# Kernel optimization log

Hardware: AMD Instinct MI355X
Metric: run time of the kernel (lower is better)

Reference implementation:

```python
import jax, jax.numpy as jnp
import numpy as np

jax.config.update("jax_enable_x64", True)  # hash arithmetic needs 64-bit ints

P = 56598313          # RzLinear.P (prime for the hash)
INPUT_DIM = 4096
OUTPUT_DIM = 4096
COMPRESS_RATIO = 0.0625
HASH_SIZE = int(INPUT_DIM * OUTPUT_DIM * COMPRESS_RATIO)  # 1,048,576
N_TOKENS = 8192


def setup_inputs() -> dict:
    key = jax.random.key(0)
    kx, kw, kr = jax.random.split(key, 3)
    x = jax.random.normal(kx, (N_TOKENS, INPUT_DIM), dtype=jnp.float32)
    hashed_weight = jax.random.normal(kw, (HASH_SIZE,), dtype=jnp.float32) * 0.02
    # _generate_random_numbers: [P, r1, r2, r3] with r_i forced even via r + r % 2
    r = jax.random.randint(kr, (3,), 0, P, dtype=jnp.int64)
    r = r + r % 2
    random_numbers = jnp.concatenate([jnp.array([P], dtype=jnp.int64), r])
    bias = jnp.zeros((OUTPUT_DIM,), dtype=jnp.float32)
    return {"x": x, "hashed_weight": hashed_weight,
            "random_numbers": random_numbers, "bias": bias}


def _hash_indices(random_numbers):
    # ROBE-Z hash (chunk_size=1): idx[k, n] = ((k*r3 + n*r2 + r1) % P) % HASH_SIZE
    r0 = random_numbers[0]
    r1 = random_numbers[1]
    r2 = random_numbers[2]
    r3 = random_numbers[3]
    k = jnp.arange(INPUT_DIM, dtype=jnp.int64)[:, None]   # (K, 1)
    n = jnp.arange(OUTPUT_DIM, dtype=jnp.int64)[None, :]  # (1, N)
    return ((k * r3 + n * r2 + r1) % r0) % HASH_SIZE       # (K, N)


def reference(x, hashed_weight, random_numbers, bias):
    idx = _hash_indices(random_numbers)
    W = hashed_weight[idx]          # gather-reconstructed (input_dim, output_dim)
    return x @ W + bias             # (N_TOKENS, output_dim)
```

## Files before the change

kernel.cpp:

```cpp
#include <hip/hip_runtime.h>
#include <stdint.h>


#define P_CONST 56598313u
#define HASH_MASK 0xFFFFFu
#define M_DIM 8192
#define N_DIM 4096
#define K_DIM 4096

typedef __attribute__((ext_vector_type(8))) short bf16x8;
typedef __attribute__((ext_vector_type(4))) float f32x4;

__device__ __forceinline__ unsigned short f2bf(float f) {
    unsigned int u = __float_as_uint(f);
    return (unsigned short)((u + 0x7FFFu + ((u >> 16) & 1u)) >> 16);
}

struct RN { unsigned long long r1, r2, r3; };

__device__ __forceinline__ RN decode_rn(const void* rn_raw) {
    RN o;
    const long long* rn64 = (const long long*)rn_raw;
    if (rn64[0] == 56598313LL) {
        o.r1 = (unsigned long long)rn64[1];
        o.r2 = (unsigned long long)rn64[2];
        o.r3 = (unsigned long long)rn64[3];
    } else {
        const int* rn32 = (const int*)rn_raw;
        o.r1 = (unsigned long long)(unsigned int)rn32[1];
        o.r2 = (unsigned long long)(unsigned int)rn32[2];
        o.r3 = (unsigned long long)(unsigned int)rn32[3];
    }
    return o;
}

__device__ __forceinline__ void load16(const void* g, void* l) {
    __builtin_amdgcn_global_load_lds(
        (const __attribute__((address_space(1))) void*)g,
        (__attribute__((address_space(3))) void*)l,
        16, 0, 0);
}

__global__ __launch_bounds__(256) void build_wt(const float* __restrict__ table,
                                                const void* __restrict__ rn_raw,
                                                unsigned short* __restrict__ Wt) {
    RN rn = decode_rn(rn_raw);
    const unsigned int stepu = (unsigned int)(rn.r3 % P_CONST);
    const unsigned int n = blockIdx.x;
    const unsigned long long base =
        ((unsigned long long)n * rn.r2 + rn.r1) % P_CONST;
    const int t = threadIdx.x;
#pragma unroll
    for (int e = 0; e < 2; ++e) {
        const int k0 = (t + e * 256) * 8;
        unsigned int cur =
            (unsigned int)((base + (unsigned long long)k0 * stepu) % P_CONST);
        union { unsigned short s[8]; uint4 v; } o;
#pragma unroll
        for (int i = 0; i < 8; ++i) {
            o.s[i] = f2bf(table[cur & HASH_MASK]);
            cur += stepu;
            if (cur >= P_CONST) cur -= P_CONST;
        }
        *(uint4*)(Wt + (size_t)n * K_DIM + k0) = o.v;
    }
}

__global__ __launch_bounds__(256) void cvt_x(const float* __restrict__ x,
                                             unsigned short* __restrict__ xb) {
    const size_t i8 = ((size_t)blockIdx.x * 256 + threadIdx.x) * 8;
    const float4 a = *(const float4*)(x + i8);
    const float4 b = *(const float4*)(x + i8 + 4);
    union { unsigned short s[8]; uint4 v; } o;
    o.s[0] = f2bf(a.x); o.s[1] = f2bf(a.y); o.s[2] = f2bf(a.z); o.s[3] = f2bf(a.w);
    o.s[4] = f2bf(b.x); o.s[5] = f2bf(b.y); o.s[6] = f2bf(b.z); o.s[7] = f2bf(b.w);
    *(uint4*)(xb + i8) = o.v;
}

__global__ __launch_bounds__(256) void gemm_bt(const unsigned short* __restrict__ A,
                                               const unsigned short* __restrict__ Bt,
                                               const float* __restrict__ bias,
                                               float* __restrict__ C) {
    __shared__ __align__(16) unsigned short lA[128 * 32];
    __shared__ __align__(16) unsigned short lB[128 * 32];
    const int t = threadIdx.x;
    const int m0 = blockIdx.y * 128;
    const int n0 = blockIdx.x * 128;
    const int lane = t & 63;
    const int w = t >> 6;
    const int wr = w >> 1, wc = w & 1;
    const int lm = lane & 15, q = lane >> 4;

    f32x4 acc[4][4] = {};

    for (int k0 = 0; k0 < K_DIM; k0 += 32) {
#pragma unroll
        for (int c = t; c < 512; c += 256) {
            const unsigned short* gp =
                A + (size_t)(m0 + (c >> 2)) * K_DIM + k0 + (c & 3) * 8;
            load16(gp, (char*)lA + (size_t)c * 16);
        }
#pragma unroll
        for (int c = t; c < 512; c += 256) {
            const unsigned short* gp =
                Bt + (size_t)(n0 + (c >> 2)) * K_DIM + k0 + (c & 3) * 8;
            load16(gp, (char*)lB + (size_t)c * 16);
        }
        __syncthreads();

        bf16x8 af[4], bfr[4];
#pragma unroll
        for (int i = 0; i < 4; ++i)
            af[i] = *(const bf16x8*)&lA[(wr * 64 + i * 16 + lm) * 32 + q * 8];
#pragma unroll
        for (int j = 0; j < 4; ++j)
            bfr[j] = *(const bf16x8*)&lB[(wc * 64 + j * 16 + lm) * 32 + q * 8];
#pragma unroll
        for (int i = 0; i < 4; ++i)
#pragma unroll
            for (int j = 0; j < 4; ++j)
                acc[i][j] = __builtin_amdgcn_mfma_f32_16x16x32_bf16(
                    af[i], bfr[j], acc[i][j], 0, 0, 0);
        __syncthreads();
    }

#pragma unroll
    for (int j = 0; j < 4; ++j) {
        const int col = n0 + wc * 64 + j * 16 + lm;
        const float bv = bias[col];
#pragma unroll
        for (int i = 0; i < 4; ++i) {
            const int row = m0 + wr * 64 + i * 16 + q * 4;
#pragma unroll
            for (int r = 0; r < 4; ++r)
                C[(size_t)(row + r) * N_DIM + col] = acc[i][j][r] + bv;
        }
    }
}

__global__ __launch_bounds__(256) void gemm_fused(const float* __restrict__ X,
                                                  const float* __restrict__ table,
                                                  const void* __restrict__ rn_raw,
                                                  const float* __restrict__ bias,
                                                  float* __restrict__ C) {
    RN rn = decode_rn(rn_raw);
    const unsigned int stepu = (unsigned int)(rn.r3 % P_CONST);
    const unsigned int step32 =
        (unsigned int)(((unsigned long long)stepu * 32ull) % P_CONST);

    __shared__ __align__(16) unsigned short lA[128 * 32];
    __shared__ __align__(16) unsigned short lB[128 * 32];
    const int t = threadIdx.x;
    const int m0 = blockIdx.y * 128;
    const int n0 = blockIdx.x * 128;
    const int lane = t & 63;
    const int w = t >> 6;
    const int wr = w >> 1, wc = w & 1;
    const int lm = lane & 15, q = lane >> 4;

    unsigned int curB[2];
    int rowB[2], colB[2];
#pragma unroll
    for (int e = 0; e < 2; ++e) {
        const int c = t + e * 256;
        rowB[e] = c >> 2;
        colB[e] = (c & 3) * 8;
        const unsigned long long base =
            ((unsigned long long)(n0 + rowB[e]) * rn.r2 + rn.r1) % P_CONST;
        curB[e] =
            (unsigned int)((base + (unsigned long long)colB[e] * stepu) % P_CONST);
    }

    f32x4 acc[4][4] = {};

    for (int k0 = 0; k0 < K_DIM; k0 += 32) {
#pragma unroll
        for (int c = t; c < 1024; c += 256) {
            const int row = c >> 3, col = (c & 7) * 4;
            const float4 v =
                *(const float4*)(X + (size_t)(m0 + row) * K_DIM + k0 + col);
            ushort4 o;
            o.x = f2bf(v.x); o.y = f2bf(v.y); o.z = f2bf(v.z); o.w = f2bf(v.w);
            *(ushort4*)&lA[row * 32 + col] = o;
        }
#pragma unroll
        for (int e = 0; e < 2; ++e) {
            unsigned int cur = curB[e];
            union { unsigned short s[8]; uint4 v; } o;
#pragma unroll
            for (int i = 0; i < 8; ++i) {
                o.s[i] = f2bf(table[cur & HASH_MASK]);
                cur += stepu;
                if (cur >= P_CONST) cur -= P_CONST;
            }
            curB[e] += step32;
            if (curB[e] >= P_CONST) curB[e] -= P_CONST;
            *(uint4*)&lB[rowB[e] * 32 + colB[e]] = o.v;
        }
        __syncthreads();

        bf16x8 af[4], bfr[4];
#pragma unroll
        for (int i = 0; i < 4; ++i)
            af[i] = *(const bf16x8*)&lA[(wr * 64 + i * 16 + lm) * 32 + q * 8];
#pragma unroll
        for (int j = 0; j < 4; ++j)
            bfr[j] = *(const bf16x8*)&lB[(wc * 64 + j * 16 + lm) * 32 + q * 8];
#pragma unroll
        for (int i = 0; i < 4; ++i)
#pragma unroll
            for (int j = 0; j < 4; ++j)
                acc[i][j] = __builtin_amdgcn_mfma_f32_16x16x32_bf16(
                    af[i], bfr[j], acc[i][j], 0, 0, 0);
        __syncthreads();
    }

#pragma unroll
    for (int j = 0; j < 4; ++j) {
        const int col = n0 + wc * 64 + j * 16 + lm;
        const float bv = bias[col];
#pragma unroll
        for (int i = 0; i < 4; ++i) {
            const int row = m0 + wr * 64 + i * 16 + q * 4;
#pragma unroll
            for (int r = 0; r < 4; ++r)
                C[(size_t)(row + r) * N_DIM + col] = acc[i][j][r] + bv;
        }
    }
}

extern "C" void kernel_launch(void* const* d_in, const int* in_sizes, int n_in,
                              void* d_out, int out_size, void* d_ws, size_t ws_size,
                              hipStream_t stream) {
    const float* x = (const float*)d_in[0];
    const float* hw = (const float*)d_in[1];
    const void* rn = d_in[2];
    const float* bias = (const float*)d_in[3];
    float* out = (float*)d_out;

    const size_t wt_bytes = (size_t)N_DIM * K_DIM * 2;
    const size_t xb_bytes = (size_t)M_DIM * K_DIM * 2;

    if (ws_size >= wt_bytes + xb_bytes) {
        unsigned short* Wt = (unsigned short*)d_ws;
        unsigned short* Xb = (unsigned short*)((char*)d_ws + wt_bytes);
        build_wt<<<N_DIM, 256, 0, stream>>>(hw, rn, Wt);
        cvt_x<<<(M_DIM * K_DIM) / (8 * 256), 256, 0, stream>>>(x, Xb);
        gemm_bt<<<dim3(N_DIM / 128, M_DIM / 128), 256, 0, stream>>>(Xb, Wt, bias, out);
    } else {
        gemm_fused<<<dim3(N_DIM / 128, M_DIM / 128), 256, 0, stream>>>(x, hw, rn, bias, out);
    }
}
```

Baseline: 591.0 us.

## Replace bf16 GEMM with 256x256-tile, 4-stage async-pipelined, swizzled LDS kernel

```diff
diff --git a/kernel.cpp b/kernel.cpp
--- a/kernel.cpp
+++ b/kernel.cpp
@@ -7,6 +7,8 @@
 #define M_DIM 8192
 #define N_DIM 4096
 #define K_DIM 4096
+#define BK 32
+#define KSTEPS (K_DIM / BK)
 
 typedef __attribute__((ext_vector_type(8))) short bf16x8;
 typedef __attribute__((ext_vector_type(4))) float f32x4;
@@ -77,10 +79,132 @@
     *(uint4*)(xb + i8) = o.v;
 }
 
-__global__ __launch_bounds__(256) void gemm_bt(const unsigned short* __restrict__ A,
-                                               const unsigned short* __restrict__ Bt,
-                                               const float* __restrict__ bias,
-                                               float* __restrict__ C) {
+__global__ __launch_bounds__(512, 2) void gemm_bt8(
+    const unsigned short* __restrict__ A,
+    const unsigned short* __restrict__ Bt,
+    const float* __restrict__ bias,
+    float* __restrict__ C) {
+    __shared__ __align__(16) unsigned short lA[4][256 * BK];
+    __shared__ __align__(16) unsigned short lB[4][256 * BK];
+
+    const int t = threadIdx.x;
+    const int bid0 = blockIdx.x;
+    const int sb = (bid0 & 7) * 64 + (bid0 >> 3);
+    const int m0 = (sb >> 4) * 256;
+    const int n0 = (sb & 15) * 256;
+
+    const int lane = t & 63;
+    const int wid = t >> 6;
+    const int wr = wid >> 2;
+    const int wc = wid & 3;
+    const int lm = lane & 15;
+    const int q = lane >> 4;
+    const int qswz = (q ^ ((lm >> 1) & 3)) << 4;
+
+    const int p0 = t * 16;
+    const int p1 = p0 + 8192;
+    const int l0 = p0 ^ ((p0 >> 3) & 0x30);
+    const int l1 = p1 ^ ((p1 >> 3) & 0x30);
+    const int r0 = l0 >> 6, c0 = (l0 & 63) >> 1;
+    const int r1 = l1 >> 6, c1 = (l1 & 63) >> 1;
+
+    const unsigned short* Abase = A + (size_t)m0 * K_DIM;
+    const unsigned short* Bbase = Bt + (size_t)n0 * K_DIM;
+
+    f32x4 acc[8][4] = {};
+
+#define STAGE_A(KS) do { const int b__ = (KS) & 3;                              \
+    load16(Abase + (size_t)r0 * K_DIM + (KS) * BK + c0, (char*)&lA[b__][0] + p0);\
+    load16(Abase + (size_t)r1 * K_DIM + (KS) * BK + c1, (char*)&lA[b__][0] + p1);\
+} while (0)
+#define STAGE_B(KS) do { const int b__ = (KS) & 3;                              \
+    load16(Bbase + (size_t)r0 * K_DIM + (KS) * BK + c0, (char*)&lB[b__][0] + p0);\
+    load16(Bbase + (size_t)r1 * K_DIM + (KS) * BK + c1, (char*)&lB[b__][0] + p1);\
+} while (0)
+
+#define STEP_BODY(KS, STG) do {                                                 \
+    __builtin_amdgcn_s_barrier();                                               \
+    asm volatile("" ::: "memory");                                              \
+    const char* bufA = (const char*)&lA[(KS) & 3][0];                           \
+    const char* bufB = (const char*)&lB[(KS) & 3][0];                           \
+    bf16x8 af[4], bfr[4];                                                       \
+    _Pragma("unroll")                                                           \
+    for (int i = 0; i < 4; ++i)                                                 \
+        af[i] = *(const bf16x8*)(bufA + (((wr * 128 + i * 16 + lm) << 6) | qswz));\
+    _Pragma("unroll")                                                           \
+    for (int j = 0; j < 4; ++j)                                                 \
+        bfr[j] = *(const bf16x8*)(bufB + (((wc * 64 + j * 16 + lm) << 6) | qswz));\
+    if (STG) STAGE_A((KS) + 3);                                                 \
+    asm volatile("s_waitcnt lgkmcnt(0)" ::: "memory");                          \
+    __builtin_amdgcn_sched_barrier(0);                                          \
+    __builtin_amdgcn_s_setprio(1);                                              \
+    _Pragma("unroll")                                                           \
+    for (int i = 0; i < 4; ++i)                                                 \
+        _Pragma("unroll")                                                       \
+        for (int j = 0; j < 4; ++j)                                             \
+            acc[i][j] = __builtin_amdgcn_mfma_f32_16x16x32_bf16(                \
+                af[i], bfr[j], acc[i][j], 0, 0, 0);                             \
+    __builtin_amdgcn_s_setprio(0);                                              \
+    __builtin_amdgcn_s_barrier();                                               \
+    asm volatile("" ::: "memory");                                              \
+    _Pragma("unroll")                                                           \
+    for (int i = 0; i < 4; ++i)                                                 \
+        af[i] = *(const bf16x8*)(bufA + (((wr * 128 + 64 + i * 16 + lm) << 6) | qswz));\
+    if (STG) STAGE_B((KS) + 3);                                                 \
+    asm volatile("s_waitcnt lgkmcnt(0)" ::: "memory");                          \
+    __builtin_amdgcn_sched_barrier(0);                                          \
+    __builtin_amdgcn_s_setprio(1);                                              \
+    _Pragma("unroll")                                                           \
+    for (int i = 0; i < 4; ++i)                                                 \
+        _Pragma("unroll")                                                       \
+        for (int j = 0; j < 4; ++j)                                             \
+            acc[i + 4][j] = __builtin_amdgcn_mfma_f32_16x16x32_bf16(            \
+                af[i], bfr[j], acc[i + 4][j], 0, 0, 0);                         \
+    __builtin_amdgcn_s_setprio(0);                                              \
+} while (0)
+
+    STAGE_A(0); STAGE_B(0);
+    STAGE_A(1); STAGE_B(1);
+    STAGE_A(2); STAGE_B(2);
+
+#pragma unroll 1
+    for (int ks = 0; ks < KSTEPS - 2; ++ks) {
+        asm volatile("s_waitcnt vmcnt(8)" ::: "memory");
+        STEP_BODY(ks, (ks < KSTEPS - 3));
+    }
+    asm volatile("s_waitcnt vmcnt(4)" ::: "memory");
+    STEP_BODY(KSTEPS - 2, false);
+    asm volatile("s_waitcnt vmcnt(0)" ::: "memory");
+    STEP_BODY(KSTEPS - 1, false);
+
+#undef STEP_BODY
+#undef STAGE_A
+#undef STAGE_B
+
+#pragma unroll
+    for (int j = 0; j < 4; ++j) {
+        const int col = n0 + wc * 64 + j * 16 + lm;
+        const float bv = bias[col];
+#pragma unroll
+        for (int i = 0; i < 8; ++i) {
+            const int row = m0 + wr * 128 + i * 16 + q * 4;
+#pragma unroll
+            for (int r = 0; r < 4; ++r)
+                C[(size_t)(row + r) * N_DIM + col] = acc[i][j][r] + bv;
+        }
+    }
+}
+
+__global__ __launch_bounds__(256) void gemm_fused(const float* __restrict__ X,
+                                                  const float* __restrict__ table,
+                                                  const void* __restrict__ rn_raw,
+                                                  const float* __restrict__ bias,
+                                                  float* __restrict__ C) {
+    RN rn = decode_rn(rn_raw);
+    const unsigned int stepu = (unsigned int)(rn.r3 % P_CONST);
+    const unsigned int step32 =
+        (unsigned int)(((unsigned long long)stepu * 32ull) % P_CONST);
+
     __shared__ __align__(16) unsigned short lA[128 * 32];
     __shared__ __align__(16) unsigned short lB[128 * 32];
     const int t = threadIdx.x;
@@ -91,73 +215,6 @@
     const int wr = w >> 1, wc = w & 1;
     const int lm = lane & 15, q = lane >> 4;
 
-    f32x4 acc[4][4] = {};
-
-    for (int k0 = 0; k0 < K_DIM; k0 += 32) {
-#pragma unroll
-        for (int c = t; c < 512; c += 256) {
-            const unsigned short* gp =
-                A + (size_t)(m0 + (c >> 2)) * K_DIM + k0 + (c & 3) * 8;
-            load16(gp, (char*)lA + (size_t)c * 16);
-        }
-#pragma unroll
-        for (int c = t; c < 512; c += 256) {
-            const unsigned short* gp =
-                Bt + (size_t)(n0 + (c >> 2)) * K_DIM + k0 + (c & 3) * 8;
-            load16(gp, (char*)lB + (size_t)c * 16);
-        }
-        __syncthreads();
-
-        bf16x8 af[4], bfr[4];
-#pragma unroll
-        for (int i = 0; i < 4; ++i)
-            af[i] = *(const bf16x8*)&lA[(wr * 64 + i * 16 + lm) * 32 + q * 8];
-#pragma unroll
-        for (int j = 0; j < 4; ++j)
-            bfr[j] = *(const bf16x8*)&lB[(wc * 64 + j * 16 + lm) * 32 + q * 8];
-#pragma unroll
-        for (int i = 0; i < 4; ++i)
-#pragma unroll
-            for (int j = 0; j < 4; ++j)
-                acc[i][j] = __builtin_amdgcn_mfma_f32_16x16x32_bf16(
-                    af[i], bfr[j], acc[i][j], 0, 0, 0);
-        __syncthreads();
-    }
-
-#pragma unroll
-    for (int j = 0; j < 4; ++j) {
-        const int col = n0 + wc * 64 + j * 16 + lm;
-        const float bv = bias[col];
-#pragma unroll
-        for (int i = 0; i < 4; ++i) {
-            const int row = m0 + wr * 64 + i * 16 + q * 4;
-#pragma unroll
-            for (int r = 0; r < 4; ++r)
-                C[(size_t)(row + r) * N_DIM + col] = acc[i][j][r] + bv;
-        }
-    }
-}
-
-__global__ __launch_bounds__(256) void gemm_fused(const float* __restrict__ X,
-                                                  const float* __restrict__ table,
-                                                  const void* __restrict__ rn_raw,
-                                                  const float* __restrict__ bias,
-                                                  float* __restrict__ C) {
-    RN rn = decode_rn(rn_raw);
-    const unsigned int stepu = (unsigned int)(rn.r3 % P_CONST);
-    const unsigned int step32 =
-        (unsigned int)(((unsigned long long)stepu * 32ull) % P_CONST);
-
-    __shared__ __align__(16) unsigned short lA[128 * 32];
-    __shared__ __align__(16) unsigned short lB[128 * 32];
-    const int t = threadIdx.x;
-    const int m0 = blockIdx.y * 128;
-    const int n0 = blockIdx.x * 128;
-    const int lane = t & 63;
-    const int w = t >> 6;
-    const int wr = w >> 1, wc = w & 1;
-    const int lm = lane & 15, q = lane >> 4;
-
     unsigned int curB[2];
     int rowB[2], colB[2];
 #pragma unroll
@@ -246,7 +303,7 @@
         unsigned short* Xb = (unsigned short*)((char*)d_ws + wt_bytes);
         build_wt<<<N_DIM, 256, 0, stream>>>(hw, rn, Wt);
         cvt_x<<<(M_DIM * K_DIM) / (8 * 256), 256, 0, stream>>>(x, Xb);
-        gemm_bt<<<dim3(N_DIM / 128, M_DIM / 128), 256, 0, stream>>>(Xb, Wt, bias, out);
+        gemm_bt8<<<dim3((M_DIM / 256) * (N_DIM / 256)), 512, 0, stream>>>(Xb, Wt, bias, out);
     } else {
         gemm_fused<<<dim3(N_DIM / 128, M_DIM / 128), 256, 0, stream>>>(x, hw, rn, bias, out);
     }
```

Result: faster. 534.7 us (-9.5%).
